# Optimization experiments

Measured on AMD Instinct MI355X. Metric: run time of the kernel, lower is better.

## Reference

```python
import jax, jax.numpy as jnp
import numpy as np
from jax import lax

T = 5        # unrolled ISTA iterations (module default)
LAM = 0.1    # soft-threshold level (module default)
B, L, K = 4096, 4096, 128


def _conv1d_same(x, k):
    """TF-style SAME cross-correlation. x: [B, L], k: [K] -> [B, L]."""
    Kw = k.shape[0]
    pad_left = (Kw - 1) // 2
    pad_right = Kw - 1 - pad_left
    out = lax.conv_general_dilated(
        x[:, None, :],            # [B, 1, L]
        k[None, None, :],         # [O=1, I=1, K]
        window_strides=(1,),
        padding=[(pad_left, pad_right)],
        dimension_numbers=("NCH", "OIH", "NCH"),
    )
    return out[:, 0, :]


def setup_inputs() -> dict:
    key = jax.random.key(0)
    k1, k2 = jax.random.split(key)
    y = jax.random.normal(k1, (B, L), dtype=jnp.float32)
    thz_pulse = jax.random.normal(k2, (K,), dtype=jnp.float32)  # learned pulse (trainable)
    step_size = jnp.full((1,), 0.1, dtype=jnp.float32)          # learned step (trainable)
    return {"y": y, "thz_pulse": thz_pulse, "step_size": step_size}


def reference(y, thz_pulse, step_size):
    x = jnp.zeros_like(y)
    h = thz_pulse           # matched-filter kernel
    h_rev = thz_pulse[::-1] # time-reversed kernel (adjoint / correlation)
    s = step_size[0]
    for _ in range(T):
        conv_out = _conv1d_same(y, h)           # H y
        residual = y - conv_out                 # y - H y
        update = _conv1d_same(residual, h_rev)  # H^T residual
        x = x + s * update                      # gradient step
        x = jnp.sign(x) * jax.nn.relu(jnp.abs(x) - LAM)  # soft-threshold
    return x
```

## Files before the change

### kernel.cpp

```cpp
#include <hip/hip_runtime.h>


typedef __bf16 bf16;
typedef __bf16 bf16x4 __attribute__((ext_vector_type(4)));
typedef __bf16 bf16x8 __attribute__((ext_vector_type(8)));
typedef float f32x4 __attribute__((ext_vector_type(4)));

#define LC 512
#define PY 824
#define PR 664
#define LAM 0.1f

__global__ __launch_bounds__(256) void ista_mfma(
    const float* __restrict__ y, const float* __restrict__ h,
    const float* __restrict__ step, float* __restrict__ out) {
  __shared__ __align__(16) bf16 ys[16 * PY];
  __shared__ __align__(16) bf16 rs[16 * PR];
  __shared__ float hs[128];

  const int tid = threadIdx.x;
  const int lane = tid & 63;
  const int wave = tid >> 6;
  const int li = lane & 15;
  const int quad = lane >> 4;
  const int chunk0 = blockIdx.x * LC;
  const int b0 = blockIdx.y * 16;

  if (tid < 128) hs[tid] = h[tid];

  {
    const int rr = tid >> 4;
    const int t = tid & 15;
    const float* yrow = y + (size_t)(b0 + rr) * 4096;
    bf16* dst = ys + rr * PY;
    for (int s4 = t; s4 < 200; s4 += 16) {
      int l = chunk0 - 128 + s4 * 4;
      float4 v;
      if (l >= 0 && l <= 4096 - 4) {
        v = *reinterpret_cast<const float4*>(yrow + l);
      } else {
        v.x = (l + 0 >= 0 && l + 0 < 4096) ? yrow[l + 0] : 0.f;
        v.y = (l + 1 >= 0 && l + 1 < 4096) ? yrow[l + 1] : 0.f;
        v.z = (l + 2 >= 0 && l + 2 < 4096) ? yrow[l + 2] : 0.f;
        v.w = (l + 3 >= 0 && l + 3 < 4096) ? yrow[l + 3] : 0.f;
      }
      bf16x4 bv;
      bv[0] = (bf16)v.x; bv[1] = (bf16)v.y; bv[2] = (bf16)v.z; bv[3] = (bf16)v.w;
      *reinterpret_cast<bf16x4*>(dst + s4 * 4) = bv;
    }
  }
  __syncthreads();

  bf16x8 A1[5], A2[5];
#pragma unroll
  for (int dd = 0; dd < 5; ++dd) {
    int d = (dd - 2) * 32;
    bf16x8 a1, a2;
#pragma unroll
    for (int j = 0; j < 8; ++j) {
      int k = quad * 8 + j;
      int idx1 = 63 + d + k - li;
      a1[j] = (idx1 >= 0 && idx1 < 128) ? (bf16)hs[idx1] : (bf16)0.f;
      int idx2 = 64 + li - d - k;
      a2[j] = (idx2 >= 0 && idx2 < 128) ? (bf16)(-hs[idx2]) : (bf16)0.f;
    }
    A1[dd] = a1; A2[dd] = a2;
  }

  for (int t = wave; t < 41; t += 4) {
    int i0 = -64 + 16 * t;
    f32x4 acc;
    {
      bf16x4 yv = *reinterpret_cast<const bf16x4*>(
          ys + li * PY + (i0 + 128) + quad * 4);
      acc[0] = -(float)yv[0]; acc[1] = -(float)yv[1];
      acc[2] = -(float)yv[2]; acc[3] = -(float)yv[3];
    }
#pragma unroll
    for (int dd = 0; dd < 5; ++dd) {
      int d = (dd - 2) * 32;
      bf16x8 bfrag = *reinterpret_cast<const bf16x8*>(
          ys + li * PY + (i0 + d + 128) + quad * 8);
      acc = __builtin_amdgcn_mfma_f32_16x16x32_bf16(A1[dd], bfrag, acc, 0, 0, 0);
    }
    bf16x4 rv;
#pragma unroll
    for (int e = 0; e < 4; ++e) {
      int g = chunk0 + i0 + quad * 4 + e;
      float v = (g >= 0 && g < 4096) ? acc[e] : 0.f;
      rv[e] = (bf16)v;
    }
    *reinterpret_cast<bf16x4*>(rs + li * PR + (i0 + 64) + quad * 4) = rv;
  }
  __syncthreads();

  const float s = step[0];
  for (int t = wave; t < 32; t += 4) {
    int i0 = 16 * t;
    f32x4 acc = {0.f, 0.f, 0.f, 0.f};
#pragma unroll
    for (int dd = 0; dd < 5; ++dd) {
      int d = (dd - 2) * 32;
      bf16x8 bfrag = *reinterpret_cast<const bf16x8*>(
          rs + li * PR + (i0 + d + 64) + quad * 8);
      acc = __builtin_amdgcn_mfma_f32_16x16x32_bf16(A2[dd], bfrag, acc, 0, 0, 0);
    }
    float4 xv;
#pragma unroll
    for (int e = 0; e < 4; ++e) {
      float su = s * acc[e];
      float x = 0.f;
#pragma unroll
      for (int it = 0; it < 5; ++it) {
        x += su;
        float ax = fabsf(x) - LAM;
        ax = ax > 0.f ? ax : 0.f;
        x = copysignf(ax, x);
      }
      (&xv.x)[e] = x;
    }
    *reinterpret_cast<float4*>(
        out + (size_t)(b0 + li) * 4096 + chunk0 + i0 + quad * 4) = xv;
  }
}

extern "C" void kernel_launch(void* const* d_in, const int* in_sizes, int n_in,
                              void* d_out, int out_size, void* d_ws,
                              size_t ws_size, hipStream_t stream) {
  const float* y = (const float*)d_in[0];
  const float* h = (const float*)d_in[1];
  const float* s = (const float*)d_in[2];
  float* out = (float*)d_out;
  ista_mfma<<<dim3(4096 / LC, 256), dim3(256), 0, stream>>>(y, h, s, out);
}
```

Baseline: 143.9 us.

## Alias residual into input LDS buffer and close-form the soft-threshold loop

Merges the separate y and residual shared-memory buffers into one smaller buffer. The residual tiles are held in registers across a barrier and then written back over the y data, which cuts LDS per block so more blocks can be resident on a CU. It also adds a launch-bounds occupancy hint, specialises the interior-chunk load and residual-masking paths, and replaces the 5-step soft-threshold loop with its closed form, sign(su)*5*max(|su|-lam,0). The cost is higher register pressure from the 11 held residual tiles plus an extra barrier.

Result: slower. 150.1 us (+4.4%).

```diff
diff --git a/kernel.cpp b/kernel.cpp
--- a/kernel.cpp
+++ b/kernel.cpp
@@ -7,15 +7,13 @@
 typedef float f32x4 __attribute__((ext_vector_type(4)));
 
 #define LC 512
-#define PY 824
-#define PR 664
+#define PY 808
 #define LAM 0.1f
 
-__global__ __launch_bounds__(256) void ista_mfma(
+__global__ __launch_bounds__(256, 4) void ista_mfma(
     const float* __restrict__ y, const float* __restrict__ h,
     const float* __restrict__ step, float* __restrict__ out) {
-  __shared__ __align__(16) bf16 ys[16 * PY];
-  __shared__ __align__(16) bf16 rs[16 * PR];
+  __shared__ __align__(16) bf16 buf[16 * PY + 64];
   __shared__ float hs[128];
 
   const int tid = threadIdx.x;
@@ -31,22 +29,29 @@
   {
     const int rr = tid >> 4;
     const int t = tid & 15;
-    const float* yrow = y + (size_t)(b0 + rr) * 4096;
-    bf16* dst = ys + rr * PY;
-    for (int s4 = t; s4 < 200; s4 += 16) {
-      int l = chunk0 - 128 + s4 * 4;
-      float4 v;
-      if (l >= 0 && l <= 4096 - 4) {
-        v = *reinterpret_cast<const float4*>(yrow + l);
-      } else {
-        v.x = (l + 0 >= 0 && l + 0 < 4096) ? yrow[l + 0] : 0.f;
-        v.y = (l + 1 >= 0 && l + 1 < 4096) ? yrow[l + 1] : 0.f;
-        v.z = (l + 2 >= 0 && l + 2 < 4096) ? yrow[l + 2] : 0.f;
-        v.w = (l + 3 >= 0 && l + 3 < 4096) ? yrow[l + 3] : 0.f;
+    const float* yrow = y + (size_t)(b0 + rr) * 4096 + (chunk0 - 128);
+    bf16* dst = buf + rr * PY;
+    if (chunk0 >= 128 && chunk0 + 672 <= 4096) {
+      for (int s4 = t; s4 < 200; s4 += 16) {
+        float4 v = *reinterpret_cast<const float4*>(yrow + s4 * 4);
+        bf16x4 bv;
+        bv[0] = (bf16)v.x; bv[1] = (bf16)v.y;
+        bv[2] = (bf16)v.z; bv[3] = (bf16)v.w;
+        *reinterpret_cast<bf16x4*>(dst + s4 * 4) = bv;
       }
-      bf16x4 bv;
-      bv[0] = (bf16)v.x; bv[1] = (bf16)v.y; bv[2] = (bf16)v.z; bv[3] = (bf16)v.w;
-      *reinterpret_cast<bf16x4*>(dst + s4 * 4) = bv;
+    } else {
+      for (int s4 = t; s4 < 200; s4 += 16) {
+        int l = chunk0 - 128 + s4 * 4;
+        float4 v;
+        v.x = (l + 0 >= 0 && l + 0 < 4096) ? yrow[s4 * 4 + 0] : 0.f;
+        v.y = (l + 1 >= 0 && l + 1 < 4096) ? yrow[s4 * 4 + 1] : 0.f;
+        v.z = (l + 2 >= 0 && l + 2 < 4096) ? yrow[s4 * 4 + 2] : 0.f;
+        v.w = (l + 3 >= 0 && l + 3 < 4096) ? yrow[s4 * 4 + 3] : 0.f;
+        bf16x4 bv;
+        bv[0] = (bf16)v.x; bv[1] = (bf16)v.y;
+        bv[2] = (bf16)v.z; bv[3] = (bf16)v.w;
+        *reinterpret_cast<bf16x4*>(dst + s4 * 4) = bv;
+      }
     }
   }
   __syncthreads();
@@ -67,57 +72,65 @@
     A1[dd] = a1; A2[dd] = a2;
   }
 
-  for (int t = wave; t < 41; t += 4) {
-    int i0 = -64 + 16 * t;
+  bf16x4 rv[11];
+  const bool edge = (chunk0 == 0) || (chunk0 + LC == 4096);
+#pragma unroll
+  for (int i = 0; i < 11; ++i) {
+    const int t = wave + 4 * i;
+    const int i0 = -64 + 16 * t;
+    const bf16* base = buf + li * PY + (i0 + 128);
     f32x4 acc;
     {
-      bf16x4 yv = *reinterpret_cast<const bf16x4*>(
-          ys + li * PY + (i0 + 128) + quad * 4);
+      bf16x4 yv = *reinterpret_cast<const bf16x4*>(base + quad * 4);
       acc[0] = -(float)yv[0]; acc[1] = -(float)yv[1];
       acc[2] = -(float)yv[2]; acc[3] = -(float)yv[3];
     }
 #pragma unroll
     for (int dd = 0; dd < 5; ++dd) {
-      int d = (dd - 2) * 32;
       bf16x8 bfrag = *reinterpret_cast<const bf16x8*>(
-          ys + li * PY + (i0 + d + 128) + quad * 8);
+          base + (dd - 2) * 32 + quad * 8);
       acc = __builtin_amdgcn_mfma_f32_16x16x32_bf16(A1[dd], bfrag, acc, 0, 0, 0);
     }
-    bf16x4 rv;
+    if (edge) {
 #pragma unroll
-    for (int e = 0; e < 4; ++e) {
-      int g = chunk0 + i0 + quad * 4 + e;
-      float v = (g >= 0 && g < 4096) ? acc[e] : 0.f;
-      rv[e] = (bf16)v;
+      for (int e = 0; e < 4; ++e) {
+        int g = chunk0 + i0 + quad * 4 + e;
+        rv[i][e] = (bf16)((g >= 0 && g < 4096) ? acc[e] : 0.f);
+      }
+    } else {
+#pragma unroll
+      for (int e = 0; e < 4; ++e) rv[i][e] = (bf16)acc[e];
     }
-    *reinterpret_cast<bf16x4*>(rs + li * PR + (i0 + 64) + quad * 4) = rv;
+  }
+  __syncthreads();
+
+#pragma unroll
+  for (int i = 0; i < 11; ++i) {
+    const int t = wave + 4 * i;
+    const int i0 = -64 + 16 * t;
+    *reinterpret_cast<bf16x4*>(buf + li * PY + (i0 + 64) + quad * 4) = rv[i];
   }
   __syncthreads();
 
   const float s = step[0];
-  for (int t = wave; t < 32; t += 4) {
-    int i0 = 16 * t;
+#pragma unroll
+  for (int i = 0; i < 8; ++i) {
+    const int t = wave + 4 * i;
+    const int i0 = 16 * t;
+    const bf16* base = buf + li * PY + (i0 + 64);
     f32x4 acc = {0.f, 0.f, 0.f, 0.f};
 #pragma unroll
     for (int dd = 0; dd < 5; ++dd) {
-      int d = (dd - 2) * 32;
       bf16x8 bfrag = *reinterpret_cast<const bf16x8*>(
-          rs + li * PR + (i0 + d + 64) + quad * 8);
+          base + (dd - 2) * 32 + quad * 8);
       acc = __builtin_amdgcn_mfma_f32_16x16x32_bf16(A2[dd], bfrag, acc, 0, 0, 0);
     }
     float4 xv;
 #pragma unroll
     for (int e = 0; e < 4; ++e) {
       float su = s * acc[e];
-      float x = 0.f;
-#pragma unroll
-      for (int it = 0; it < 5; ++it) {
-        x += su;
-        float ax = fabsf(x) - LAM;
-        ax = ax > 0.f ? ax : 0.f;
-        x = copysignf(ax, x);
-      }
-      (&xv.x)[e] = x;
+      float ax = fmaxf(fabsf(su) - LAM, 0.f);
+      (&xv.x)[e] = copysignf(5.f * ax, su);
     }
     *reinterpret_cast<float4*>(
         out + (size_t)(b0 + li) * 4096 + chunk0 + i0 + quad * 4) = xv;
```
